# Kernel tuning notes

Measured on AMD Instinct MI355X. Metric: run time of the kernel, lower is better.

Reference implementation:

```python
import jax, jax.numpy as jnp
import numpy as np

BN_EPS = 1e-5


def _spe_forward(feature, neigh_idx, W, gamma, beta, running_mean, running_var):
    # feature: [B, C, N, 1]; neigh_idx: [B, N, K]
    B = feature.shape[0]
    pc = jnp.transpose(feature[..., 0], (0, 2, 1))            # [B, N, C]
    # gather neighbor features: [B, N, K, C]
    f_neigh = pc[jnp.arange(B)[:, None, None], neigh_idx]
    f_neigh = jnp.transpose(f_neigh, (0, 3, 1, 2))            # [B, C, N, K]
    f = jnp.concatenate((feature, f_neigh), axis=-1)          # [B, C, N, K+1]
    # 1x1 conv (no bias, followed by BN)
    h = jnp.einsum('oc,bcnk->bonk', W, f)                     # [B, O, N, K+1]
    # BatchNorm2d (eval mode with running stats) + ReLU
    inv = gamma / jnp.sqrt(running_var + BN_EPS)
    h = h * inv[None, :, None, None] + (beta - running_mean * inv)[None, :, None, None]
    h = jax.nn.relu(h)
    # sum over the neighbor axis, keepdim
    return jnp.sum(h, axis=-1, keepdims=True)                 # [B, O, N, 1]


def setup_inputs() -> dict:
    key = jax.random.key(0)
    k1, k2, k3 = jax.random.split(key, 3)
    B, C, N, K, O = 2, 64, 32768, 16, 64
    feature = jax.random.normal(k1, (B, C, N, 1), dtype=jnp.float32)
    neigh_idx = jax.random.randint(k2, (B, N, K), 0, N, dtype=jnp.int32)
    W = jax.random.normal(k3, (O, C), dtype=jnp.float32) * (1.0 / np.sqrt(C))
    gamma = jnp.ones((O,), dtype=jnp.float32)
    beta = jnp.zeros((O,), dtype=jnp.float32)
    running_mean = jnp.zeros((O,), dtype=jnp.float32)
    running_var = jnp.ones((O,), dtype=jnp.float32)
    return {"feature": feature, "neigh_idx": neigh_idx, "W": W,
            "gamma": gamma, "beta": beta,
            "running_mean": running_mean, "running_var": running_var}


def reference(feature, neigh_idx, W, gamma, beta, running_mean, running_var):
    return _spe_forward(feature, neigh_idx, W, gamma, beta, running_mean, running_var)
```

## Files before the change

kernel.cpp:

```cpp
#include <hip/hip_runtime.h>

#define BN_EPS 1e-5f

constexpr int Bb = 2;
constexpr int Cc = 64;
constexpr int Nn = 32768;
constexpr int Kk = 16;
constexpr int Oo = 64;

typedef __attribute__((ext_vector_type(8))) short v8s;
typedef __attribute__((ext_vector_type(4))) float v4f;

__device__ __forceinline__ unsigned short f2bf(float f) {
    unsigned u = __float_as_uint(f);
    return (unsigned short)((u + 0x7FFFu + ((u >> 16) & 1u)) >> 16);
}

__global__ __launch_bounds__(1024) void spe_gemm_mfma(
    const float* __restrict__ feature, const float* __restrict__ W,
    const float* __restrict__ gamma, const float* __restrict__ beta,
    const float* __restrict__ rmean, const float* __restrict__ rvar,
    unsigned short* __restrict__ t)
{
    __shared__ unsigned short Wl[64][68];
    __shared__ float invs[64], biass[64];
    const int tid = threadIdx.x;
    const int blk = blockIdx.x;
    const int b   = blk & 1;
    const int n0  = (blk >> 1) << 8;

    #pragma unroll
    for (int j = 0; j < 4; ++j) {
        const int i = j * 1024 + tid;
        Wl[i >> 6][i & 63] = f2bf(W[i]);
    }
    if (tid < 64) {
        const float iv = gamma[tid] / sqrtf(rvar[tid] + BN_EPS);
        invs[tid]  = iv;
        biass[tid] = beta[tid] - rmean[tid] * iv;
    }

    const int wv   = tid >> 6;
    const int lane = tid & 63;
    const int q    = lane >> 4;
    const int r16  = lane & 15;

    union U { ushort4 u4[2]; unsigned short us[8]; v8s v; };

    const int nb = n0 + wv * 16 + r16;
    const float* fp = feature + (size_t)b * Cc * Nn + nb;
    U bf0, bf1;
    #pragma unroll
    for (int jj = 0; jj < 8; ++jj) {
        bf0.us[jj] = f2bf(fp[(size_t)(q * 8 + jj) * Nn]);
        bf1.us[jj] = f2bf(fp[(size_t)(q * 8 + jj + 32) * Nn]);
    }
    __syncthreads();

    #pragma unroll
    for (int ot = 0; ot < 4; ++ot) {
        const int oa = ot * 16 + r16;
        U af0, af1;
        af0.u4[0] = *(const ushort4*)&Wl[oa][q * 8];
        af0.u4[1] = *(const ushort4*)&Wl[oa][q * 8 + 4];
        af1.u4[0] = *(const ushort4*)&Wl[oa][q * 8 + 32];
        af1.u4[1] = *(const ushort4*)&Wl[oa][q * 8 + 36];

        v4f c = {0.f, 0.f, 0.f, 0.f};
        c = __builtin_amdgcn_mfma_f32_16x16x32_bf16(af0.v, bf0.v, c, 0, 0, 0);
        c = __builtin_amdgcn_mfma_f32_16x16x32_bf16(af1.v, bf1.v, c, 0, 0, 0);

        const int ob4 = ot * 16 + q * 4;
        const float4 iv4 = *(const float4*)&invs[ob4];
        const float4 bi4 = *(const float4*)&biass[ob4];

        ushort4 ov;
        ov.x = f2bf(fmaxf(fmaf(iv4.x, c[0], bi4.x), 0.0f));
        ov.y = f2bf(fmaxf(fmaf(iv4.y, c[1], bi4.y), 0.0f));
        ov.z = f2bf(fmaxf(fmaf(iv4.z, c[2], bi4.z), 0.0f));
        ov.w = f2bf(fmaxf(fmaf(iv4.w, c[3], bi4.w), 0.0f));
        *(ushort4*)&t[((size_t)b * Nn + nb) * 64 + ob4] = ov;
    }
}

__global__ __launch_bounds__(512, 2) void spe_gather_sum(
    const unsigned short* __restrict__ t, const int* __restrict__ idx,
    float* __restrict__ out)
{
    __shared__ float s[64 * 65];
    const int tid  = threadIdx.x;
    const int wv   = tid >> 6;
    const int lane = tid & 63;
    const int p    = lane >> 3;
    const int e    = lane & 7;
    const int blk  = blockIdx.x;
    const int b    = blk & 1;
    const int n0   = (blk >> 1) << 6;
    const int ng   = n0 + wv * 8;

    const unsigned short* tb = t + (size_t)b * Nn * 64;

    const int2 mi = ((const int2*)(idx + ((size_t)b * Nn + ng) * Kk))[lane];

    int nj[16];
    #pragma unroll
    for (int j = 0; j < 16; ++j)
        nj[j] = __shfl((j & 1) ? mi.y : mi.x, p * 8 + (j >> 1));

    uint4 v[17];
    v[0] = *(const uint4*)&tb[(size_t)(ng + p) * 64 + e * 8];
    #pragma unroll
    for (int j = 0; j < 16; ++j)
        v[j + 1] = *(const uint4*)&tb[(size_t)nj[j] * 64 + e * 8];

    float acc[8] = {0.f, 0.f, 0.f, 0.f, 0.f, 0.f, 0.f, 0.f};
    #pragma unroll
    for (int j = 0; j < 17; ++j) {
        acc[0] += __uint_as_float(v[j].x << 16);
        acc[1] += __uint_as_float(v[j].x & 0xFFFF0000u);
        acc[2] += __uint_as_float(v[j].y << 16);
        acc[3] += __uint_as_float(v[j].y & 0xFFFF0000u);
        acc[4] += __uint_as_float(v[j].z << 16);
        acc[5] += __uint_as_float(v[j].z & 0xFFFF0000u);
        acc[6] += __uint_as_float(v[j].w << 16);
        acc[7] += __uint_as_float(v[j].w & 0xFFFF0000u);
    }

    float* sp = &s[(wv * 8 + p) * 65 + e * 8];
    #pragma unroll
    for (int i = 0; i < 8; ++i) sp[i] = acc[i];
    __syncthreads();

    const int nl2 = tid & 63;
    const int ob  = tid >> 6;
    float* op = out + (size_t)b * Oo * Nn + n0 + nl2;
    #pragma unroll
    for (int i = 0; i < 8; ++i) {
        const int o = ob * 8 + i;
        op[(size_t)o * Nn] = s[nl2 * 65 + o];
    }
}

extern "C" void kernel_launch(void* const* d_in, const int* in_sizes, int n_in,
                              void* d_out, int out_size, void* d_ws, size_t ws_size,
                              hipStream_t stream) {
    const float* feature = (const float*)d_in[0];
    const int*   nidx    = (const int*)d_in[1];
    const float* W       = (const float*)d_in[2];
    const float* gamma   = (const float*)d_in[3];
    const float* beta    = (const float*)d_in[4];
    const float* rmean   = (const float*)d_in[5];
    const float* rvar    = (const float*)d_in[6];
    float* out = (float*)d_out;
    unsigned short* t = (unsigned short*)d_ws;

    spe_gemm_mfma<<<Bb * (Nn / 256), 1024, 0, stream>>>(feature, W, gamma, beta, rmean, rvar, t);
    spe_gather_sum<<<Bb * (Nn / 64), 512, 0, stream>>>(t, nidx, out);
}
```

Before: 95.00 us.

## Split intermediate into channel halves and gather each half in separate passes

The GEMM kernel now writes its bf16 output as two 32-channel planes instead of one 64-channel row per point. The gather kernel is launched twice, once per half, so each pass randomly reads 64-byte rows from a 4 MB table that fits in cache better. The gather also uses nontemporal index loads and vectorized nontemporal float4 output stores, with higher occupancy bounds. In exchange, the index array is read twice and random accesses become smaller 8-byte-per-lane transactions.

```diff
diff --git a/kernel.cpp b/kernel.cpp
--- a/kernel.cpp
+++ b/kernel.cpp
@@ -10,6 +10,7 @@
 
 typedef __attribute__((ext_vector_type(8))) short v8s;
 typedef __attribute__((ext_vector_type(4))) float v4f;
+typedef __attribute__((ext_vector_type(2))) int   v2i;
 
 __device__ __forceinline__ unsigned short f2bf(float f) {
     unsigned u = __float_as_uint(f);
@@ -79,15 +80,17 @@
         ov.y = f2bf(fmaxf(fmaf(iv4.y, c[1], bi4.y), 0.0f));
         ov.z = f2bf(fmaxf(fmaf(iv4.z, c[2], bi4.z), 0.0f));
         ov.w = f2bf(fmaxf(fmaf(iv4.w, c[3], bi4.w), 0.0f));
-        *(ushort4*)&t[((size_t)b * Nn + nb) * 64 + ob4] = ov;
+        const int h = ob4 >> 5;
+        *(ushort4*)&t[((size_t)(h * 2 + b) * Nn + nb) * 32 + (ob4 & 31)] = ov;
     }
 }
 
-__global__ __launch_bounds__(512, 2) void spe_gather_sum(
-    const unsigned short* __restrict__ t, const int* __restrict__ idx,
-    float* __restrict__ out)
+__global__ __launch_bounds__(512, 4) void spe_gather_half(
+    const unsigned short* __restrict__ th,
+    const int* __restrict__ idx,
+    float* __restrict__ out, const int oB)
 {
-    __shared__ float s[64 * 65];
+    __shared__ float s[64 * 33];
     const int tid  = threadIdx.x;
     const int wv   = tid >> 6;
     const int lane = tid & 63;
@@ -98,47 +101,45 @@
     const int n0   = (blk >> 1) << 6;
     const int ng   = n0 + wv * 8;
 
-    const unsigned short* tb = t + (size_t)b * Nn * 64;
+    const unsigned short* tb = th + (size_t)b * Nn * 32;
 
-    const int2 mi = ((const int2*)(idx + ((size_t)b * Nn + ng) * Kk))[lane];
+    const v2i mi = __builtin_nontemporal_load(
+        (const v2i*)(idx + ((size_t)b * Nn + ng) * Kk) + lane);
 
     int nj[16];
     #pragma unroll
     for (int j = 0; j < 16; ++j)
-        nj[j] = __shfl((j & 1) ? mi.y : mi.x, p * 8 + (j >> 1));
+        nj[j] = __shfl(mi[j & 1], p * 8 + (j >> 1));
 
-    uint4 v[17];
-    v[0] = *(const uint4*)&tb[(size_t)(ng + p) * 64 + e * 8];
+    uint2 v[17];
+    v[0] = *(const uint2*)&tb[(size_t)(ng + p) * 32 + e * 4];
     #pragma unroll
     for (int j = 0; j < 16; ++j)
-        v[j + 1] = *(const uint4*)&tb[(size_t)nj[j] * 64 + e * 8];
+        v[j + 1] = *(const uint2*)&tb[(size_t)nj[j] * 32 + e * 4];
 
-    float acc[8] = {0.f, 0.f, 0.f, 0.f, 0.f, 0.f, 0.f, 0.f};
+    float acc[4] = {0.f, 0.f, 0.f, 0.f};
     #pragma unroll
     for (int j = 0; j < 17; ++j) {
         acc[0] += __uint_as_float(v[j].x << 16);
         acc[1] += __uint_as_float(v[j].x & 0xFFFF0000u);
         acc[2] += __uint_as_float(v[j].y << 16);
         acc[3] += __uint_as_float(v[j].y & 0xFFFF0000u);
-        acc[4] += __uint_as_float(v[j].z << 16);
-        acc[5] += __uint_as_float(v[j].z & 0xFFFF0000u);
-        acc[6] += __uint_as_float(v[j].w << 16);
-        acc[7] += __uint_as_float(v[j].w & 0xFFFF0000u);
     }
 
-    float* sp = &s[(wv * 8 + p) * 65 + e * 8];
+    float* sp = &s[(wv * 8 + p) * 33 + e * 4];
     #pragma unroll
-    for (int i = 0; i < 8; ++i) sp[i] = acc[i];
+    for (int i = 0; i < 4; ++i) sp[i] = acc[i];
     __syncthreads();
 
-    const int nl2 = tid & 63;
-    const int ob  = tid >> 6;
-    float* op = out + (size_t)b * Oo * Nn + n0 + nl2;
-    #pragma unroll
-    for (int i = 0; i < 8; ++i) {
-        const int o = ob * 8 + i;
-        op[(size_t)o * Nn] = s[nl2 * 65 + o];
-    }
+    const int o  = tid >> 4;
+    const int g  = tid & 15;
+    v4f val;
+    val[0] = s[(g * 4 + 0) * 33 + o];
+    val[1] = s[(g * 4 + 1) * 33 + o];
+    val[2] = s[(g * 4 + 2) * 33 + o];
+    val[3] = s[(g * 4 + 3) * 33 + o];
+    __builtin_nontemporal_store(val,
+        (v4f*)&out[((size_t)b * Oo + oB + o) * Nn + n0 + g * 4]);
 }
 
 extern "C" void kernel_launch(void* const* d_in, const int* in_sizes, int n_in,
@@ -155,5 +156,7 @@
     unsigned short* t = (unsigned short*)d_ws;
 
     spe_gemm_mfma<<<Bb * (Nn / 256), 1024, 0, stream>>>(feature, W, gamma, beta, rmean, rvar, t);
-    spe_gather_sum<<<Bb * (Nn / 64), 512, 0, stream>>>(t, nidx, out);
+    const size_t regionElems = (size_t)Bb * Nn * 32;
+    spe_gather_half<<<Bb * (Nn / 64), 512, 0, stream>>>(t,               nidx, out,  0);
+    spe_gather_half<<<Bb * (Nn / 64), 512, 0, stream>>>(t + regionElems, nidx, out, 32);
 }
```

After: 101.8 us. 1.07x slower.

## Fuse GEMM and gather-sum into one cooperative kernel with grid sync

Applied to the files above, without the earlier changes.

Merges the MFMA projection kernel and the neighbor gather-sum kernel into a single cooperative launch of 256 blocks, separated by a grid-wide barrier, so the second launch and its gap disappear. Each block now handles 256 points in the gather phase, split into two passes of 128, and writes output with vectorized nontemporal float4 stores. Index loads also become nontemporal. The cost is a grid sync, a larger shared-memory footprint, and only 256 blocks of 1024 threads for the gather phase, which may lower occupancy for this latency-bound random gather.

```diff
diff --git a/kernel.cpp b/kernel.cpp
--- a/kernel.cpp
+++ b/kernel.cpp
@@ -1,4 +1,5 @@
 #include <hip/hip_runtime.h>
+#include <hip/hip_cooperative_groups.h>
 
 #define BN_EPS 1e-5f
 
@@ -10,134 +11,144 @@
 
 typedef __attribute__((ext_vector_type(8))) short v8s;
 typedef __attribute__((ext_vector_type(4))) float v4f;
+typedef __attribute__((ext_vector_type(2))) int   v2i;
 
 __device__ __forceinline__ unsigned short f2bf(float f) {
     unsigned u = __float_as_uint(f);
     return (unsigned short)((u + 0x7FFFu + ((u >> 16) & 1u)) >> 16);
 }
 
-__global__ __launch_bounds__(1024) void spe_gemm_mfma(
-    const float* __restrict__ feature, const float* __restrict__ W,
+__global__ __launch_bounds__(1024) void spe_fused(
+    const float* __restrict__ feature, const int* __restrict__ idx,
+    const float* __restrict__ W,
     const float* __restrict__ gamma, const float* __restrict__ beta,
     const float* __restrict__ rmean, const float* __restrict__ rvar,
-    unsigned short* __restrict__ t)
+    float* __restrict__ out, unsigned short* __restrict__ t)
 {
     __shared__ unsigned short Wl[64][68];
     __shared__ float invs[64], biass[64];
+    __shared__ float s[128 * 65];
+
     const int tid = threadIdx.x;
     const int blk = blockIdx.x;
     const int b   = blk & 1;
     const int n0  = (blk >> 1) << 8;
 
-    #pragma unroll
-    for (int j = 0; j < 4; ++j) {
-        const int i = j * 1024 + tid;
-        Wl[i >> 6][i & 63] = f2bf(W[i]);
-    }
-    if (tid < 64) {
-        const float iv = gamma[tid] / sqrtf(rvar[tid] + BN_EPS);
-        invs[tid]  = iv;
-        biass[tid] = beta[tid] - rmean[tid] * iv;
+    const int wv   = tid >> 6;
+    const int lane = tid & 63;
+
+    {
+        #pragma unroll
+        for (int j = 0; j < 4; ++j) {
+            const int i = j * 1024 + tid;
+            Wl[i >> 6][i & 63] = f2bf(W[i]);
+        }
+        if (tid < 64) {
+            const float iv = gamma[tid] / sqrtf(rvar[tid] + BN_EPS);
+            invs[tid]  = iv;
+            biass[tid] = beta[tid] - rmean[tid] * iv;
+        }
+
+        const int q   = lane >> 4;
+        const int r16 = lane & 15;
+
+        union U { ushort4 u4[2]; unsigned short us[8]; v8s v; };
+
+        const int nb = n0 + wv * 16 + r16;
+        const float* fp = feature + (size_t)b * Cc * Nn + nb;
+        U bf0, bf1;
+        #pragma unroll
+        for (int jj = 0; jj < 8; ++jj) {
+            bf0.us[jj] = f2bf(fp[(size_t)(q * 8 + jj) * Nn]);
+            bf1.us[jj] = f2bf(fp[(size_t)(q * 8 + jj + 32) * Nn]);
+        }
+        __syncthreads();
+
+        #pragma unroll
+        for (int ot = 0; ot < 4; ++ot) {
+            const int oa = ot * 16 + r16;
+            U af0, af1;
+            af0.u4[0] = *(const ushort4*)&Wl[oa][q * 8];
+            af0.u4[1] = *(const ushort4*)&Wl[oa][q * 8 + 4];
+            af1.u4[0] = *(const ushort4*)&Wl[oa][q * 8 + 32];
+            af1.u4[1] = *(const ushort4*)&Wl[oa][q * 8 + 36];
+
+            v4f c = {0.f, 0.f, 0.f, 0.f};
+            c = __builtin_amdgcn_mfma_f32_16x16x32_bf16(af0.v, bf0.v, c, 0, 0, 0);
+            c = __builtin_amdgcn_mfma_f32_16x16x32_bf16(af1.v, bf1.v, c, 0, 0, 0);
+
+            const int ob4 = ot * 16 + q * 4;
+            const float4 iv4 = *(const float4*)&invs[ob4];
+            const float4 bi4 = *(const float4*)&biass[ob4];
+
+            ushort4 ov;
+            ov.x = f2bf(fmaxf(fmaf(iv4.x, c[0], bi4.x), 0.0f));
+            ov.y = f2bf(fmaxf(fmaf(iv4.y, c[1], bi4.y), 0.0f));
+            ov.z = f2bf(fmaxf(fmaf(iv4.z, c[2], bi4.z), 0.0f));
+            ov.w = f2bf(fmaxf(fmaf(iv4.w, c[3], bi4.w), 0.0f));
+            *(ushort4*)&t[((size_t)b * Nn + nb) * 64 + ob4] = ov;
+        }
     }
 
-    const int wv   = tid >> 6;
-    const int lane = tid & 63;
-    const int q    = lane >> 4;
-    const int r16  = lane & 15;
+    cooperative_groups::this_grid().sync();
 
-    union U { ushort4 u4[2]; unsigned short us[8]; v8s v; };
+    {
+        const unsigned short* tb = t + (size_t)b * Nn * 64;
+        const int p = lane >> 3;
+        const int e = lane & 7;
 
-    const int nb = n0 + wv * 16 + r16;
-    const float* fp = feature + (size_t)b * Cc * Nn + nb;
-    U bf0, bf1;
-    #pragma unroll
-    for (int jj = 0; jj < 8; ++jj) {
-        bf0.us[jj] = f2bf(fp[(size_t)(q * 8 + jj) * Nn]);
-        bf1.us[jj] = f2bf(fp[(size_t)(q * 8 + jj + 32) * Nn]);
-    }
-    __syncthreads();
+        #pragma unroll
+        for (int np = 0; np < 2; ++np) {
+            const int nbase = n0 + np * 128;
+            const int ng    = nbase + wv * 8;
 
-    #pragma unroll
-    for (int ot = 0; ot < 4; ++ot) {
-        const int oa = ot * 16 + r16;
-        U af0, af1;
-        af0.u4[0] = *(const ushort4*)&Wl[oa][q * 8];
-        af0.u4[1] = *(const ushort4*)&Wl[oa][q * 8 + 4];
-        af1.u4[0] = *(const ushort4*)&Wl[oa][q * 8 + 32];
-        af1.u4[1] = *(const ushort4*)&Wl[oa][q * 8 + 36];
+            const v2i mi = __builtin_nontemporal_load(
+                (const v2i*)(idx + ((size_t)b * Nn + ng) * Kk) + lane);
 
-        v4f c = {0.f, 0.f, 0.f, 0.f};
-        c = __builtin_amdgcn_mfma_f32_16x16x32_bf16(af0.v, bf0.v, c, 0, 0, 0);
-        c = __builtin_amdgcn_mfma_f32_16x16x32_bf16(af1.v, bf1.v, c, 0, 0, 0);
+            int nj[16];
+            #pragma unroll
+            for (int j = 0; j < 16; ++j)
+                nj[j] = __shfl(mi[j & 1], p * 8 + (j >> 1));
 
-        const int ob4 = ot * 16 + q * 4;
-        const float4 iv4 = *(const float4*)&invs[ob4];
-        const float4 bi4 = *(const float4*)&biass[ob4];
+            uint4 v[17];
+            v[0] = *(const uint4*)&tb[(size_t)(ng + p) * 64 + e * 8];
+            #pragma unroll
+            for (int j = 0; j < 16; ++j)
+                v[j + 1] = *(const uint4*)&tb[(size_t)nj[j] * 64 + e * 8];
 
-        ushort4 ov;
-        ov.x = f2bf(fmaxf(fmaf(iv4.x, c[0], bi4.x), 0.0f));
-        ov.y = f2bf(fmaxf(fmaf(iv4.y, c[1], bi4.y), 0.0f));
-        ov.z = f2bf(fmaxf(fmaf(iv4.z, c[2], bi4.z), 0.0f));
-        ov.w = f2bf(fmaxf(fmaf(iv4.w, c[3], bi4.w), 0.0f));
-        *(ushort4*)&t[((size_t)b * Nn + nb) * 64 + ob4] = ov;
-    }
-}
+            float acc[8] = {0.f, 0.f, 0.f, 0.f, 0.f, 0.f, 0.f, 0.f};
+            #pragma unroll
+            for (int j = 0; j < 17; ++j) {
+                acc[0] += __uint_as_float(v[j].x << 16);
+                acc[1] += __uint_as_float(v[j].x & 0xFFFF0000u);
+                acc[2] += __uint_as_float(v[j].y << 16);
+                acc[3] += __uint_as_float(v[j].y & 0xFFFF0000u);
+                acc[4] += __uint_as_float(v[j].z << 16);
+                acc[5] += __uint_as_float(v[j].z & 0xFFFF0000u);
+                acc[6] += __uint_as_float(v[j].w << 16);
+                acc[7] += __uint_as_float(v[j].w & 0xFFFF0000u);
+            }
 
-__global__ __launch_bounds__(512, 2) void spe_gather_sum(
-    const unsigned short* __restrict__ t, const int* __restrict__ idx,
-    float* __restrict__ out)
-{
-    __shared__ float s[64 * 65];
-    const int tid  = threadIdx.x;
-    const int wv   = tid >> 6;
-    const int lane = tid & 63;
-    const int p    = lane >> 3;
-    const int e    = lane & 7;
-    const int blk  = blockIdx.x;
-    const int b    = blk & 1;
-    const int n0   = (blk >> 1) << 6;
-    const int ng   = n0 + wv * 8;
+            float* sp = &s[(wv * 8 + p) * 65 + e * 8];
+            #pragma unroll
+            for (int i = 0; i < 8; ++i) sp[i] = acc[i];
+            __syncthreads();
 
-    const unsigned short* tb = t + (size_t)b * Nn * 64;
-
-    const int2 mi = ((const int2*)(idx + ((size_t)b * Nn + ng) * Kk))[lane];
-
-    int nj[16];
-    #pragma unroll
-    for (int j = 0; j < 16; ++j)
-        nj[j] = __shfl((j & 1) ? mi.y : mi.x, p * 8 + (j >> 1));
-
-    uint4 v[17];
-    v[0] = *(const uint4*)&tb[(size_t)(ng + p) * 64 + e * 8];
-    #pragma unroll
-    for (int j = 0; j < 16; ++j)
-        v[j + 1] = *(const uint4*)&tb[(size_t)nj[j] * 64 + e * 8];
-
-    float acc[8] = {0.f, 0.f, 0.f, 0.f, 0.f, 0.f, 0.f, 0.f};
-    #pragma unroll
-    for (int j = 0; j < 17; ++j) {
-        acc[0] += __uint_as_float(v[j].x << 16);
-        acc[1] += __uint_as_float(v[j].x & 0xFFFF0000u);
-        acc[2] += __uint_as_float(v[j].y << 16);
-        acc[3] += __uint_as_float(v[j].y & 0xFFFF0000u);
-        acc[4] += __uint_as_float(v[j].z << 16);
-        acc[5] += __uint_as_float(v[j].z & 0xFFFF0000u);
-        acc[6] += __uint_as_float(v[j].w << 16);
-        acc[7] += __uint_as_float(v[j].w & 0xFFFF0000u);
-    }
-
-    float* sp = &s[(wv * 8 + p) * 65 + e * 8];
-    #pragma unroll
-    for (int i = 0; i < 8; ++i) sp[i] = acc[i];
-    __syncthreads();
-
-    const int nl2 = tid & 63;
-    const int ob  = tid >> 6;
-    float* op = out + (size_t)b * Oo * Nn + n0 + nl2;
-    #pragma unroll
-    for (int i = 0; i < 8; ++i) {
-        const int o = ob * 8 + i;
-        op[(size_t)o * Nn] = s[nl2 * 65 + o];
+            #pragma unroll
+            for (int i = 0; i < 2; ++i) {
+                const int o    = tid >> 4;
+                const int g    = tid & 15;
+                const int nloc = i * 64 + g * 4;
+                v4f val;
+                val[0] = s[(nloc + 0) * 65 + o];
+                val[1] = s[(nloc + 1) * 65 + o];
+                val[2] = s[(nloc + 2) * 65 + o];
+                val[3] = s[(nloc + 3) * 65 + o];
+                __builtin_nontemporal_store(val,
+                    (v4f*)&out[((size_t)b * Oo + o) * Nn + nbase + nloc]);
+            }
+            __syncthreads();
+        }
     }
 }
 
@@ -154,6 +165,9 @@
     float* out = (float*)d_out;
     unsigned short* t = (unsigned short*)d_ws;
 
-    spe_gemm_mfma<<<Bb * (Nn / 256), 1024, 0, stream>>>(feature, W, gamma, beta, rmean, rvar, t);
-    spe_gather_sum<<<Bb * (Nn / 64), 512, 0, stream>>>(t, nidx, out);
+    void* args[] = {(void*)&feature, (void*)&nidx, (void*)&W, (void*)&gamma,
+                    (void*)&beta, (void*)&rmean, (void*)&rvar,
+                    (void*)&out, (void*)&t};
+    hipLaunchCooperativeKernel((const void*)spe_fused, dim3(256), dim3(1024),
+                               args, 0, stream);
 }
```

Result: slower. 140.0 us (+47.4%).
